# Kernel tuning notes

Measured on AMD Instinct MI355X. Metric: run time of the kernel, lower is better.

Reference implementation:

```python
import jax, jax.numpy as jnp
from jax import lax
import numpy as np

SEQ, BATCH, IN, HID = 512, 64, 300, 512
G = 4 * HID  # gate dim, torch order: i, f, g, o


def setup_inputs() -> dict:
    key = jax.random.key(0)
    k1, k2, k3, k4, k5 = jax.random.split(key, 5)
    s = 1.0 / np.sqrt(HID)
    return {
        "inputs": jax.random.normal(k1, (SEQ, BATCH, IN), dtype=jnp.float32),
        "W_ih": jax.random.normal(k2, (G, IN), dtype=jnp.float32) * s,
        "W_hh": jax.random.normal(k3, (G, HID), dtype=jnp.float32) * s,
        "b_ih": jax.random.normal(k4, (G,), dtype=jnp.float32) * s,
        "b_hh": jax.random.normal(k5, (G,), dtype=jnp.float32) * s,
    }


def reference(inputs, W_ih, W_hh, b_ih, b_hh):
    # Encoder: zero-init state, single-layer unidirectional LSTM (W/A bits = 32
    # -> full-precision math), return final hidden state reshaped [batch, -1].
    B = inputs.shape[1]
    H = W_hh.shape[1]
    # Precompute input projection for all timesteps: [T, B, 4H]
    x_proj = jnp.einsum('tbi,gi->tbg', inputs, W_ih) + b_ih + b_hh

    def step(carry, xp_t):
        h, c = carry
        gates = xp_t + h @ W_hh.T  # [B, 4H]
        i, f, g, o = jnp.split(gates, 4, axis=-1)
        i = jax.nn.sigmoid(i)
        f = jax.nn.sigmoid(f)
        g = jnp.tanh(g)
        o = jax.nn.sigmoid(o)
        c = f * c + i * g
        h = o * jnp.tanh(c)
        return (h, c), h

    h0 = jnp.zeros((B, H), dtype=inputs.dtype)
    (ht, ct), _ = lax.scan(step, (h0, h0), x_proj)
    # n_cells=1, birnn=False -> ht.view(batch, -1) == ht
    return ht
```

## Files before the change

### kernel.cpp

```cpp
#include <hip/hip_runtime.h>


typedef float  f32x4  __attribute__((ext_vector_type(4)));
typedef __bf16 bf16x8 __attribute__((ext_vector_type(8)));
typedef unsigned short u16x4 __attribute__((ext_vector_type(4)));

#define TSEQ 512
#define INDIM 300
#define HID 512

#define OWH 0
#define OWI 65536
#define OH  106496
#define OX  122880
#define ORED 133120
#define LDSZ 137472

__device__ __forceinline__ unsigned short f2bf(float f) {
    union { float f; unsigned u; } v; v.f = f;
    unsigned r = v.u + 0x7fffu + ((v.u >> 16) & 1u);
    return (unsigned short)(r >> 16);
}
__device__ __forceinline__ float fsigmoid(float x) {
    return 1.0f / (1.0f + __expf(-x));
}
__device__ __forceinline__ float ftanh(float x) {
    float e = __expf(2.0f * x);
    return 1.0f - 2.0f / (e + 1.0f);
}

extern "C" __global__ __launch_bounds__(256, 1) void lstm_fused(
    const float* __restrict__ inputs,
    const float* __restrict__ Wih,
    const float* __restrict__ Whh,
    const float* __restrict__ bih,
    const float* __restrict__ bhh,
    unsigned int* __restrict__ hcomm,
    float* __restrict__ out)
{
    __shared__ __align__(16) char lds[LDSZ];

    const int tid = threadIdx.x;
    const int wg  = blockIdx.x;
    const int grp = wg & 7;
    const int mw  = wg >> 3;

    {
        f32x4 z = {0.0f, 0.0f, 0.0f, 0.0f};
        for (int n = 0; n < 17; ++n) {
            int i = n * 256 + tid;
            if (i < 4224)
                *reinterpret_cast<f32x4*>(lds + OWI + i * 16) = z;
        }
    }
    __syncthreads();

    for (int n = 0; n < 32; ++n) {
        int i  = n * 256 + tid;
        int r  = i >> 7;
        int ic = i & 127;
        int q = r >> 4, jj = r & 15;
        const float4 w = *reinterpret_cast<const float4*>(
            Whh + ((size_t)(q * HID + mw * 16 + jj) * HID + ic * 4));
        u16x4 p = {f2bf(w.x), f2bf(w.y), f2bf(w.z), f2bf(w.w)};
        *reinterpret_cast<u16x4*>(lds + OWH + r * 1024 +
                                  ((ic * 8) ^ ((r & 7) << 4))) = p;
    }
    for (int n = 0; n < 19; ++n) {
        int i = n * 256 + tid;
        if (i < 4800) {
            int r  = i / 75;
            int ic = i - r * 75;
            int q = r >> 4, jj = r & 15;
            const float4 w = *reinterpret_cast<const float4*>(
                Wih + ((size_t)(q * HID + mw * 16 + jj) * INDIM + ic * 4));
            u16x4 p = {f2bf(w.x), f2bf(w.y), f2bf(w.z), f2bf(w.w)};
            *reinterpret_cast<u16x4*>(lds + OWI + r * 640 +
                                      ((ic * 8) ^ ((r & 7) << 4))) = p;
        }
    }

    const int lane = tid & 63;
    const int wv   = tid >> 6;
    const int arow = wv * 16 + (lane & 15);
    const int kb16 = (lane >> 4) << 4;
    const int amask = (arow & 7) << 4;
    const int aoffh = arow * 1024;
    const int aoffi = arow * 640;
    const int bcol  = lane & 15;
    const int bmask = (bcol & 7) << 4;
    const int boffh = bcol * 1024;
    const int boffi = bcol * 640;

    const int aj = tid & 15;
    const int ab = tid >> 4;
    float bias0 = 0.f, bias1 = 0.f, bias2 = 0.f, bias3 = 0.f;
    if (tid < 128) {
        int hidx = mw * 16 + aj;
        bias0 = bih[0 * HID + hidx] + bhh[0 * HID + hidx];
        bias1 = bih[1 * HID + hidx] + bhh[1 * HID + hidx];
        bias2 = bih[2 * HID + hidx] + bhh[2 * HID + hidx];
        bias3 = bih[3 * HID + hidx] + bhh[3 * HID + hidx];
    }
    float cst = 0.0f;

    float* red = reinterpret_cast<float*>(lds + ORED);

    __syncthreads();

#pragma unroll 1
    for (int t = 0; t < TSEQ; ++t) {
#pragma unroll
        for (int n = 0; n < 3; ++n) {
            int i = n * 256 + tid;
            if (i < 600) {
                int b  = i / 75;
                int ic = i - b * 75;
                const float4 v = *reinterpret_cast<const float4*>(
                    inputs + ((size_t)t * 64 + grp * 8 + b) * INDIM + ic * 4);
                u16x4 p = {f2bf(v.x), f2bf(v.y), f2bf(v.z), f2bf(v.w)};
                *reinterpret_cast<u16x4*>(lds + OX + b * 640 +
                                          ((ic * 8) ^ ((b & 7) << 4))) = p;
            }
        }
        __syncthreads();

        unsigned long long hv64[8];
        const unsigned long long* hc = reinterpret_cast<const unsigned long long*>(
            hcomm + (size_t)(t & 1) * 32768) + (size_t)grp * 2048 + tid;
        if (t > 0) {
#pragma unroll
            for (int b = 0; b < 8; ++b)
                hv64[b] = __hip_atomic_load(hc + b * 256, __ATOMIC_RELAXED,
                                            __HIP_MEMORY_SCOPE_AGENT);
        }

        f32x4 acc0 = {0.f, 0.f, 0.f, 0.f};
        f32x4 acc1 = {0.f, 0.f, 0.f, 0.f};
#pragma unroll
        for (int m = 0; m < 10; ++m) {
            bf16x8 a = *reinterpret_cast<const bf16x8*>(
                lds + OWI + aoffi + ((m * 64 + kb16) ^ amask));
            bf16x8 b = *reinterpret_cast<const bf16x8*>(
                lds + OX + boffi + ((m * 64 + kb16) ^ bmask));
            if (m & 1) acc1 = __builtin_amdgcn_mfma_f32_16x16x32_bf16(a, b, acc1, 0, 0, 0);
            else       acc0 = __builtin_amdgcn_mfma_f32_16x16x32_bf16(a, b, acc0, 0, 0, 0);
        }

        if (t > 0) {
            const unsigned long long expect =
                ((unsigned long long)t << 48) | ((unsigned long long)t << 16);
            const unsigned long long tmask = 0xffff0000ffff0000ull;
#pragma unroll
            for (int b = 0; b < 8; ++b) {
                while ((hv64[b] & tmask) != expect) {
                    __builtin_amdgcn_s_sleep(1);
                    hv64[b] = __hip_atomic_load(hc + b * 256, __ATOMIC_RELAXED,
                                                __HIP_MEMORY_SCOPE_AGENT);
                }
                unsigned pk = (unsigned)(hv64[b] & 0xffffu) |
                              ((unsigned)((hv64[b] >> 32) & 0xffffu) << 16);
                *reinterpret_cast<unsigned*>(
                    lds + OH + b * 1024 + ((tid * 4) ^ ((b & 7) << 4))) = pk;
            }
        }
        __syncthreads();

        if (t > 0) {
#pragma unroll
            for (int m = 0; m < 16; ++m) {
                bf16x8 a = *reinterpret_cast<const bf16x8*>(
                    lds + OWH + aoffh + ((m * 64 + kb16) ^ amask));
                bf16x8 b = *reinterpret_cast<const bf16x8*>(
                    lds + OH + boffh + ((m * 64 + kb16) ^ bmask));
                if (m & 1) acc1 = __builtin_amdgcn_mfma_f32_16x16x32_bf16(a, b, acc1, 0, 0, 0);
                else       acc0 = __builtin_amdgcn_mfma_f32_16x16x32_bf16(a, b, acc0, 0, 0, 0);
            }
        }
        f32x4 accv = acc0 + acc1;

        {
            int rbase = (wv * 16 + ((lane >> 4) << 2)) * 17 + bcol;
            red[rbase + 0]  = accv.x;
            red[rbase + 17] = accv.y;
            red[rbase + 34] = accv.z;
            red[rbase + 51] = accv.w;
        }
        __syncthreads();

        if (tid < 128) {
            float gi = bias0 + red[(0 * 16 + aj) * 17 + ab];
            float gf = bias1 + red[(1 * 16 + aj) * 17 + ab];
            float gg = bias2 + red[(2 * 16 + aj) * 17 + ab];
            float go = bias3 + red[(3 * 16 + aj) * 17 + ab];
            float ig = fsigmoid(gi);
            float fg = fsigmoid(gf);
            float cg = ftanh(gg);
            float og = fsigmoid(go);
            cst = fg * cst + ig * cg;
            float hv = og * ftanh(cst);
            if (t == TSEQ - 1) {
                out[(size_t)(grp * 8 + ab) * HID + mw * 16 + aj] = hv;
            } else {
                unsigned word = ((unsigned)(t + 1) << 16) | (unsigned)f2bf(hv);
                __hip_atomic_store(
                    hcomm + (size_t)((t + 1) & 1) * 32768 +
                        (size_t)(grp * 8 + ab) * 512 + mw * 16 + aj,
                    word, __ATOMIC_RELAXED, __HIP_MEMORY_SCOPE_AGENT);
            }
        }
        __syncthreads();
    }
}

extern "C" void kernel_launch(void* const* d_in, const int* in_sizes, int n_in,
                              void* d_out, int out_size, void* d_ws, size_t ws_size,
                              hipStream_t stream) {
    const float* inputs = (const float*)d_in[0];
    const float* Wih    = (const float*)d_in[1];
    const float* Whh    = (const float*)d_in[2];
    const float* bih    = (const float*)d_in[3];
    const float* bhh    = (const float*)d_in[4];
    float* out = (float*)d_out;

    unsigned int* hcomm = (unsigned int*)d_ws;

    hipMemsetAsync(hcomm, 0, 2 * 64 * 512 * sizeof(unsigned int), stream);

    void* args[] = {(void*)&inputs, (void*)&Wih, (void*)&Whh, (void*)&bih,
                    (void*)&bhh,    (void*)&hcomm, (void*)&out};
    hipLaunchCooperativeKernel(reinterpret_cast<void*>(lstm_fused),
                               dim3(256), dim3(256), args, 0, stream);
}
```

Before: 1.263 ms.

## Double-buffer input tiles and reduction buffer, prefetch next step, drop barriers

Prefetches the next timestep's input slice into registers during the current step and writes it into an alternate LDS buffer, so the global input load leaves the critical recurrent path. The reduction scratch is double-buffered too, which allows removing the step-start and step-end barriers. The h-spin wait now polls all pending words together without s_sleep instead of spinning on each one serially. This costs extra LDS and register pressure, and the busy polling adds memory traffic.

```diff
diff --git a/kernel.cpp b/kernel.cpp
--- a/kernel.cpp
+++ b/kernel.cpp
@@ -4,6 +4,7 @@
 typedef float  f32x4  __attribute__((ext_vector_type(4)));
 typedef __bf16 bf16x8 __attribute__((ext_vector_type(8)));
 typedef unsigned short u16x4 __attribute__((ext_vector_type(4)));
+typedef unsigned long long u64;
 
 #define TSEQ 512
 #define INDIM 300
@@ -12,9 +13,11 @@
 #define OWH 0
 #define OWI 65536
 #define OH  106496
-#define OX  122880
-#define ORED 133120
-#define LDSZ 137472
+#define OX0 122880
+#define OX1 133120
+#define ORED0 143360
+#define ORED1 147712
+#define LDSZ 152064
 
 __device__ __forceinline__ unsigned short f2bf(float f) {
     union { float f; unsigned u; } v; v.f = f;
@@ -47,10 +50,9 @@
 
     {
         f32x4 z = {0.0f, 0.0f, 0.0f, 0.0f};
-        for (int n = 0; n < 17; ++n) {
+        for (int n = 0; n < 19; ++n) {
             int i = n * 256 + tid;
-            if (i < 4224)
-                *reinterpret_cast<f32x4*>(lds + OWI + i * 16) = z;
+            *reinterpret_cast<f32x4*>(lds + OWI + i * 16) = z;
         }
     }
     __syncthreads();
@@ -104,29 +106,34 @@
     }
     float cst = 0.0f;
 
-    float* red = reinterpret_cast<float*>(lds + ORED);
-
+    const int i0 = tid,      b0 = i0 / 75, c0 = i0 - b0 * 75;
+    const int i1 = 256 + tid, b1 = i1 / 75, c1 = i1 - b1 * 75;
+    const int i2 = 512 + tid, b2 = i2 / 75, c2 = i2 - b2 * 75;
+    const bool has2 = (i2 < 600);
+
+    {
+        const float* xb = inputs + (size_t)(grp * 8) * INDIM;
+        float4 v0 = *reinterpret_cast<const float4*>(xb + (size_t)b0 * INDIM + c0 * 4);
+        float4 v1 = *reinterpret_cast<const float4*>(xb + (size_t)b1 * INDIM + c1 * 4);
+        u16x4 p0 = {f2bf(v0.x), f2bf(v0.y), f2bf(v0.z), f2bf(v0.w)};
+        u16x4 p1 = {f2bf(v1.x), f2bf(v1.y), f2bf(v1.z), f2bf(v1.w)};
+        *reinterpret_cast<u16x4*>(lds + OX0 + b0 * 640 + ((c0 * 8) ^ ((b0 & 7) << 4))) = p0;
+        *reinterpret_cast<u16x4*>(lds + OX0 + b1 * 640 + ((c1 * 8) ^ ((b1 & 7) << 4))) = p1;
+        if (has2) {
+            float4 v2 = *reinterpret_cast<const float4*>(xb + (size_t)b2 * INDIM + c2 * 4);
+            u16x4 p2 = {f2bf(v2.x), f2bf(v2.y), f2bf(v2.z), f2bf(v2.w)};
+            *reinterpret_cast<u16x4*>(lds + OX0 + b2 * 640 + ((c2 * 8) ^ ((b2 & 7) << 4))) = p2;
+        }
+    }
     __syncthreads();
 
 #pragma unroll 1
     for (int t = 0; t < TSEQ; ++t) {
-#pragma unroll
-        for (int n = 0; n < 3; ++n) {
-            int i = n * 256 + tid;
-            if (i < 600) {
-                int b  = i / 75;
-                int ic = i - b * 75;
-                const float4 v = *reinterpret_cast<const float4*>(
-                    inputs + ((size_t)t * 64 + grp * 8 + b) * INDIM + ic * 4);
-                u16x4 p = {f2bf(v.x), f2bf(v.y), f2bf(v.z), f2bf(v.w)};
-                *reinterpret_cast<u16x4*>(lds + OX + b * 640 +
-                                          ((ic * 8) ^ ((b & 7) << 4))) = p;
-            }
-        }
-        __syncthreads();
-
-        unsigned long long hv64[8];
-        const unsigned long long* hc = reinterpret_cast<const unsigned long long*>(
+        const char* oxc = lds + OX0 + (t & 1) * 10240;
+        float* red = reinterpret_cast<float*>(lds + ORED0 + (t & 1) * 4352);
+
+        u64 hv64[8];
+        const u64* hc = reinterpret_cast<const u64*>(
             hcomm + (size_t)(t & 1) * 32768) + (size_t)grp * 2048 + tid;
         if (t > 0) {
 #pragma unroll
@@ -142,22 +149,39 @@
             bf16x8 a = *reinterpret_cast<const bf16x8*>(
                 lds + OWI + aoffi + ((m * 64 + kb16) ^ amask));
             bf16x8 b = *reinterpret_cast<const bf16x8*>(
-                lds + OX + boffi + ((m * 64 + kb16) ^ bmask));
+                oxc + boffi + ((m * 64 + kb16) ^ bmask));
             if (m & 1) acc1 = __builtin_amdgcn_mfma_f32_16x16x32_bf16(a, b, acc1, 0, 0, 0);
             else       acc0 = __builtin_amdgcn_mfma_f32_16x16x32_bf16(a, b, acc0, 0, 0, 0);
         }
 
+        float4 xv0, xv1, xv2;
+        if (t + 1 < TSEQ) {
+            const float* xb = inputs + ((size_t)(t + 1) * 64 + grp * 8) * INDIM;
+            xv0 = *reinterpret_cast<const float4*>(xb + (size_t)b0 * INDIM + c0 * 4);
+            xv1 = *reinterpret_cast<const float4*>(xb + (size_t)b1 * INDIM + c1 * 4);
+            if (has2)
+                xv2 = *reinterpret_cast<const float4*>(xb + (size_t)b2 * INDIM + c2 * 4);
+        }
+
         if (t > 0) {
-            const unsigned long long expect =
-                ((unsigned long long)t << 48) | ((unsigned long long)t << 16);
-            const unsigned long long tmask = 0xffff0000ffff0000ull;
+            const u64 expect = ((u64)t << 48) | ((u64)t << 16);
+            const u64 tmask  = 0xffff0000ffff0000ull;
+            unsigned pend = 0;
+#pragma unroll
+            for (int b = 0; b < 8; ++b)
+                if ((hv64[b] & tmask) != expect) pend |= 1u << b;
+            while (pend) {
+#pragma unroll
+                for (int b = 0; b < 8; ++b)
+                    if (pend & (1u << b))
+                        hv64[b] = __hip_atomic_load(hc + b * 256, __ATOMIC_RELAXED,
+                                                    __HIP_MEMORY_SCOPE_AGENT);
+#pragma unroll
+                for (int b = 0; b < 8; ++b)
+                    if ((hv64[b] & tmask) == expect) pend &= ~(1u << b);
+            }
 #pragma unroll
             for (int b = 0; b < 8; ++b) {
-                while ((hv64[b] & tmask) != expect) {
-                    __builtin_amdgcn_s_sleep(1);
-                    hv64[b] = __hip_atomic_load(hc + b * 256, __ATOMIC_RELAXED,
-                                                __HIP_MEMORY_SCOPE_AGENT);
-                }
                 unsigned pk = (unsigned)(hv64[b] & 0xffffu) |
                               ((unsigned)((hv64[b] >> 32) & 0xffffu) << 16);
                 *reinterpret_cast<unsigned*>(
@@ -178,6 +202,18 @@
             }
         }
         f32x4 accv = acc0 + acc1;
+
+        if (t + 1 < TSEQ) {
+            char* oxn = lds + OX0 + ((t + 1) & 1) * 10240;
+            u16x4 p0 = {f2bf(xv0.x), f2bf(xv0.y), f2bf(xv0.z), f2bf(xv0.w)};
+            u16x4 p1 = {f2bf(xv1.x), f2bf(xv1.y), f2bf(xv1.z), f2bf(xv1.w)};
+            *reinterpret_cast<u16x4*>(oxn + b0 * 640 + ((c0 * 8) ^ ((b0 & 7) << 4))) = p0;
+            *reinterpret_cast<u16x4*>(oxn + b1 * 640 + ((c1 * 8) ^ ((b1 & 7) << 4))) = p1;
+            if (has2) {
+                u16x4 p2 = {f2bf(xv2.x), f2bf(xv2.y), f2bf(xv2.z), f2bf(xv2.w)};
+                *reinterpret_cast<u16x4*>(oxn + b2 * 640 + ((c2 * 8) ^ ((b2 & 7) << 4))) = p2;
+            }
+        }
 
         {
             int rbase = (wv * 16 + ((lane >> 4) << 2)) * 17 + bcol;
@@ -209,7 +245,6 @@
                     word, __ATOMIC_RELAXED, __HIP_MEMORY_SCOPE_AGENT);
             }
         }
-        __syncthreads();
     }
 }
 
```

New measurement: 1.650 ms. 1.31x slower.
